# Kernel tuning notes

Measured on AMD Instinct MI355X. Metric: run time of the kernel, lower is better.

Reference implementation:

```python
import jax, jax.numpy as jnp
import numpy as np

N_NODES = 20000
IN_CH = 512
HEADS = 8
CH = 64  # hidden_layer per head
E = 320000
E_LABEL = 100000


def setup_inputs() -> dict:
    key = jax.random.key(0)
    ks = jax.random.split(key, 8)
    x = jax.random.normal(ks[0], (N_NODES, IN_CH), dtype=jnp.float32)
    edge_index = jax.random.randint(ks[1], (2, E), 0, N_NODES)
    edge_label_index = jax.random.randint(ks[2], (2, E_LABEL), 0, N_NODES)
    # GATv2Conv params (share_weights=False, bias=True)
    sc = 1.0 / np.sqrt(IN_CH)
    W_l = jax.random.normal(ks[3], (IN_CH, HEADS * CH), dtype=jnp.float32) * sc
    W_r = jax.random.normal(ks[4], (IN_CH, HEADS * CH), dtype=jnp.float32) * sc
    att = jax.random.normal(ks[5], (HEADS, CH), dtype=jnp.float32) * (1.0 / np.sqrt(CH))
    bias = jnp.zeros((HEADS * CH,), dtype=jnp.float32)
    gamma = jnp.ones((HEADS * CH,), dtype=jnp.float32)
    beta = jnp.zeros((HEADS * CH,), dtype=jnp.float32)
    return {"x": x, "edge_index": edge_index, "edge_label_index": edge_label_index,
            "W_l": W_l, "W_r": W_r, "att": att, "bias": bias,
            "gamma": gamma, "beta": beta}


def reference(x, edge_index, edge_label_index, W_l, W_r, att, bias, gamma, beta):
    N = x.shape[0]
    H, C = att.shape
    src, dst = edge_index[0], edge_index[1]
    # GATv2Conv: separate source/target linear maps
    xl = (x @ W_l).reshape(N, H, C)
    xr = (x @ W_r).reshape(N, H, C)
    # per-edge attention logits (GATv2: leaky_relu BEFORE attention vector)
    e = jax.nn.leaky_relu(xl[src] + xr[dst], negative_slope=0.2)  # [E,H,C]
    alpha = jnp.einsum('ehc,hc->eh', e, att)                      # [E,H]
    # softmax over incoming edges of each destination node
    amax = jax.ops.segment_max(alpha, dst, num_segments=N)        # [N,H]
    alpha = jnp.exp(alpha - amax[dst])
    denom = jax.ops.segment_sum(alpha, dst, num_segments=N)       # [N,H]
    alpha = alpha / (denom[dst] + 1e-16)
    # scatter-add aggregation of attended source messages
    out = jax.ops.segment_sum(alpha[:, :, None] * xl[src], dst, num_segments=N)  # [N,H,C]
    out = out.reshape(N, H * C) + bias
    # BatchNorm1d (training-mode batch stats, eps=1e-5)
    mu = out.mean(axis=0)
    var = out.var(axis=0)
    out = (out - mu) * jax.lax.rsqrt(var + 1e-5) * gamma + beta
    out = jax.nn.relu(out)  # dropout is identity in deterministic reference
    # gather + dot-product link scoring
    s = out[edge_label_index[0]]
    t = out[edge_label_index[1]]
    return jnp.sum(s * t, axis=1)  # [E_LABEL]
```

## Files before the change

kernel.cpp:

```cpp
#include <hip/hip_runtime.h>
#include <hip/hip_bf16.h>
#include <cstdint>

#define IN_CH 512
#define HC    512
#define HEADS 8
#define NPACK 1024

typedef __attribute__((ext_vector_type(8))) short bf16x8;
typedef __attribute__((ext_vector_type(8))) ushort u16x8;
typedef __attribute__((ext_vector_type(4))) float f32x4;
typedef __attribute__((ext_vector_type(2))) float f32x2;
typedef const __attribute__((address_space(1))) uint8_t* gaddr_t;
typedef __attribute__((address_space(3))) uint8_t* laddr_t;

__device__ inline ushort f2bf(float f) {
  uint32_t u = __float_as_uint(f);
  return (ushort)((u + 0x7fffu + ((u >> 16) & 1u)) >> 16);
}
__device__ inline float bf2f(ushort u) {
  return __uint_as_float(((uint32_t)u) << 16);
}

#if defined(__has_builtin)
#if __has_builtin(__builtin_amdgcn_cvt_pk_f32_fp8) && __has_builtin(__builtin_amdgcn_cvt_pk_fp8_f32)
#define HAVE_HW_FP8 1
#endif
#endif

__device__ __forceinline__ float fp8_decode_sw(uint32_t v) {
  const uint32_t t = v & 0x7fu;
  float m;
  if (t >= 8u) m = __uint_as_float((((t >> 3) + 120u) << 23) | ((t & 7u) << 20));
  else m = (float)t * 0.001953125f;
  return (v & 0x80u) ? -m : m;
}
__device__ __forceinline__ uint8_t fp8_encode_sw(float f) {
  const uint32_t b = __float_as_uint(f);
  const uint32_t s = (b >> 24) & 0x80u;
  uint32_t a = b & 0x7fffffffu;
  if (a >= 0x43e00000u) return (uint8_t)(s | 0x7eu);
  if (a < 0x3c800000u) {
    const int qi = (int)(__uint_as_float(a) * 512.0f + 0.5f);
    return (uint8_t)(s | (qi >= 8 ? 8u : (uint32_t)qi));
  }
  const uint32_t r = a + 0x7ffffu + ((a >> 20) & 1u);
  const uint32_t e = r >> 23;
  if (e > 135u) return (uint8_t)(s | 0x7eu);
  return (uint8_t)(s | ((e - 120u) << 3) | ((r >> 20) & 7u));
}

__device__ __forceinline__ void fp8x2_to_f32(uint32_t u, float& f0, float& f1, bool hi) {
#ifdef HAVE_HW_FP8
  const f32x2 p = hi ? __builtin_amdgcn_cvt_pk_f32_fp8(u, true)
                     : __builtin_amdgcn_cvt_pk_f32_fp8(u, false);
  f0 = p.x; f1 = p.y;
#else
  const uint32_t w = hi ? (u >> 16) : u;
  f0 = fp8_decode_sw(w & 0xffu);
  f1 = fp8_decode_sw((w >> 8) & 0xffu);
#endif
}
__device__ __forceinline__ uint8_t f32_to_fp8(float f) {
#ifdef HAVE_HW_FP8
  return (uint8_t)(__builtin_amdgcn_cvt_pk_fp8_f32(f, f, 0, false) & 0xff);
#else
  return fp8_encode_sw(f);
#endif
}

template<int CTRL>
__device__ __forceinline__ float dpp_add(float s) {
  const int t = __builtin_amdgcn_update_dpp(0, __float_as_int(s), CTRL, 0xf, 0xf, true);
  return s + __int_as_float(t);
}

__global__ void prep(const float* __restrict__ x, ushort* __restrict__ xb,
                     const float* __restrict__ Wl, const float* __restrict__ Wr,
                     ushort* __restrict__ bt,
                     const int* __restrict__ ei, int* __restrict__ counts,
                     const int* __restrict__ eli, int* __restrict__ counts2,
                     int n4, int E, int EL, int nbc, int nbp, int nbh) {
  const int b = blockIdx.x;
  if (b < nbc) {
    const int i = b * 256 + threadIdx.x;
    if (i < n4) {
      const float4 v = ((const float4*)x)[i];
      ushort4 o;
      o.x = f2bf(v.x); o.y = f2bf(v.y); o.z = f2bf(v.z); o.w = f2bf(v.w);
      ((ushort4*)xb)[i] = o;
    }
  } else if (b < nbc + nbp) {
    const int i = (b - nbc) * 256 + threadIdx.x;
    if (i < NPACK * IN_CH) {
      const int n = i >> 9, k = i & 511;
      const float v = (n < HC) ? Wl[(size_t)k * HC + n] : Wr[(size_t)k * HC + (n - HC)];
      bt[i] = f2bf(v);
    }
  } else if (b < nbc + nbp + nbh) {
    const int e = (b - nbc - nbp) * 256 + threadIdx.x;
    if (e < E) atomicAdd(&counts[ei[E + e]], 1);
  } else {
    const int e = (b - nbc - nbp - nbh) * 256 + threadIdx.x;
    if (e < EL) atomicAdd(&counts2[eli[e]], 1);
  }
}

__global__ __launch_bounds__(256) void gemm_mfma(
    const ushort* __restrict__ xb, const ushort* __restrict__ bt,
    uint8_t* __restrict__ xl8, ushort* __restrict__ xrb, int M) {
  __shared__ __align__(16) ushort As[128 * 32];
  __shared__ __align__(16) ushort Bs[128 * 32];
  const int wave = threadIdx.x >> 6, lane = threadIdx.x & 63;
  const int row0 = blockIdx.y * 128, col0 = blockIdx.x * 128;
  const int quad = lane >> 4, m16 = lane & 15;
  const int wrow = (wave >> 1) * 64, wcol = (wave & 1) * 64;
  const int srow = lane >> 2;
  const int scol = (lane & 3) * 8;
  const f32x4 zero = {0.f, 0.f, 0.f, 0.f};
  f32x4 acc[4][4];
  #pragma unroll
  for (int i = 0; i < 4; ++i)
    #pragma unroll
    for (int j = 0; j < 4; ++j) acc[i][j] = zero;

  for (int k0 = 0; k0 < IN_CH; k0 += 32) {
    #pragma unroll
    for (int c = 0; c < 2; ++c) {
      const int chunk = wave * 2 + c;
      const ushort* ga = xb + (size_t)(row0 + chunk * 16 + srow) * IN_CH + k0 + scol;
      __builtin_amdgcn_global_load_lds((gaddr_t)ga, (laddr_t)(As + chunk * 512), 16, 0, 0);
      const ushort* gb = bt + (size_t)(col0 + chunk * 16 + srow) * IN_CH + k0 + scol;
      __builtin_amdgcn_global_load_lds((gaddr_t)gb, (laddr_t)(Bs + chunk * 512), 16, 0, 0);
    }
    __syncthreads();
    bf16x8 af[4], bfr[4];
    #pragma unroll
    for (int i = 0; i < 4; ++i)
      af[i] = *(const bf16x8*)(As + (wrow + i * 16 + m16) * 32 + quad * 8);
    #pragma unroll
    for (int j = 0; j < 4; ++j)
      bfr[j] = *(const bf16x8*)(Bs + (wcol + j * 16 + m16) * 32 + quad * 8);
    #pragma unroll
    for (int i = 0; i < 4; ++i)
      #pragma unroll
      for (int j = 0; j < 4; ++j)
        acc[i][j] = __builtin_amdgcn_mfma_f32_16x16x32_bf16(af[i], bfr[j], acc[i][j], 0, 0, 0);
    __syncthreads();
  }
  const bool isL = (col0 < HC);
  if (isL) {
    #pragma unroll
    for (int i = 0; i < 4; ++i) {
      const int r = row0 + wrow + i * 16 + quad * 4;
      #pragma unroll
      for (int j = 0; j < 4; ++j) {
        const int cg = col0 + wcol + j * 16 + m16;
        #pragma unroll
        for (int t = 0; t < 4; ++t) {
          const int rr = r + t;
          if (rr < M) xl8[(size_t)rr * HC + cg] = f32_to_fp8(acc[i][j][t]);
        }
      }
    }
  } else {
    const int cbase = col0 - HC;
    #pragma unroll
    for (int i = 0; i < 4; ++i) {
      const int r = row0 + wrow + i * 16 + quad * 4;
      #pragma unroll
      for (int j = 0; j < 4; ++j) {
        const int cg = cbase + wcol + j * 16 + m16;
        #pragma unroll
        for (int t = 0; t < 4; ++t) {
          const int rr = r + t;
          if (rr < M) xrb[(size_t)rr * HC + cg] = f2bf(acc[i][j][t]);
        }
      }
    }
  }
}

__global__ __launch_bounds__(256) void scan_fused(
    const int* __restrict__ cA, int* __restrict__ oA, int* __restrict__ curA,
    int* __restrict__ fA,
    const int* __restrict__ cB, int* __restrict__ oB, int* __restrict__ curB,
    int* __restrict__ fB, int Nn, int nb) {
  const int half = (blockIdx.x >= nb) ? 1 : 0;
  const int blk  = blockIdx.x - half * nb;
  const int* counts = half ? cB : cA;
  int* offsets = half ? oB : oA;
  int* cursor  = half ? curB : curA;
  int* flags   = half ? fB : fA;
  __shared__ int tmp[256];
  __shared__ int sPref;
  const int t = threadIdx.x;
  const int i = blk * 256 + t;
  const int v = (i < Nn) ? counts[i] : 0;
  tmp[t] = v;
  __syncthreads();
  for (int d = 1; d < 256; d <<= 1) {
    int add = (t >= d) ? tmp[t - d] : 0;
    __syncthreads();
    tmp[t] += add;
    __syncthreads();
  }
  if (t == 0) atomicExch(&flags[blk], tmp[255] + 1);
  if (t < 64) {
    int s = 0;
    for (int b = t; b < blk; b += 64) {
      int f;
      do { f = atomicOr(&flags[b], 0); } while (f == 0);
      s += f - 1;
    }
    #pragma unroll
    for (int off = 32; off > 0; off >>= 1) s += __shfl_down(s, off, 64);
    if (t == 0) sPref = s;
  }
  __syncthreads();
  const int pref = sPref;
  if (i < Nn) {
    const int o = tmp[t] - v + pref;
    offsets[i] = o;
    cursor[i] = o;
  }
}

__global__ void csr_fill(const int* __restrict__ ei, int* __restrict__ cursor,
                         int* __restrict__ csr_src,
                         const int* __restrict__ eli, int* __restrict__ cursor2,
                         int* __restrict__ csr_t, int* __restrict__ csr_eid,
                         int E, int EL, int nbE) {
  const int b = blockIdx.x;
  if (b < nbE) {
    const int e = b * 256 + threadIdx.x;
    if (e < E) {
      const int pos = atomicAdd(&cursor[ei[E + e]], 1);
      csr_src[pos] = ei[e];
    }
  } else {
    const int e = (b - nbE) * 256 + threadIdx.x;
    if (e < EL) {
      const int pos = atomicAdd(&cursor2[eli[e]], 1);
      csr_t[pos] = eli[EL + e];
      csr_eid[pos] = e;
    }
  }
}

__global__ __launch_bounds__(256) void gatv2_agg(
    const uint8_t* __restrict__ xl8, const ushort* xrb, const float* __restrict__ att,
    const int* __restrict__ offsets, const int* __restrict__ counts,
    const int* __restrict__ csr_src, ushort* agg, int Nn) {
  const int node = blockIdx.x * 4 + (threadIdx.x >> 6);
  const int lane = threadIdx.x & 63;
  if (node >= Nn) return;
  const int start = offsets[node];
  const int deg   = counts[node];
  float rv[8], tv[8];
  {
    const u16x8 ur = *(const u16x8*)(xrb + (size_t)node * HC + lane * 8);
    #pragma unroll
    for (int c = 0; c < 8; ++c) rv[c] = bf2f((ushort)ur[c]);
    const float4* pa = (const float4*)(att + lane * 8);
    const float4 t0 = pa[0], t1 = pa[1];
    tv[0]=t0.x; tv[1]=t0.y; tv[2]=t0.z; tv[3]=t0.w;
    tv[4]=t1.x; tv[5]=t1.y; tv[6]=t1.z; tv[7]=t1.w;
  }
  float acc[8] = {};
  float densum = 0.f;
  const int* ps = csr_src + start;
  auto row = [&](int idx) {
    return *(const uint2*)(xl8 + (size_t)ps[idx] * HC + lane * 8);
  };
  auto body = [&](const uint2 cur) {
    float a[8];
    fp8x2_to_f32(cur.x, a[0], a[1], false);
    fp8x2_to_f32(cur.x, a[2], a[3], true);
    fp8x2_to_f32(cur.y, a[4], a[5], false);
    fp8x2_to_f32(cur.y, a[6], a[7], true);
    float s0 = 0.f, s1 = 0.f;
    #pragma unroll
    for (int c = 0; c < 4; ++c) {
      const float v = a[c] + rv[c];
      s0 += fmaxf(v, 0.2f * v) * tv[c];
    }
    #pragma unroll
    for (int c = 4; c < 8; ++c) {
      const float v = a[c] + rv[c];
      s1 += fmaxf(v, 0.2f * v) * tv[c];
    }
    float s = s0 + s1;
    s = dpp_add<0xB1>(s);
    s = dpp_add<0x4E>(s);
    s = dpp_add<0x141>(s);
    const float ea = __expf(s);
    densum += ea;
    #pragma unroll
    for (int c = 0; c < 8; ++c) acc[c] += ea * a[c];
  };

  uint2 b0 = {}, b1 = {};
  if (deg > 0) b0 = row(0);
  if (deg > 1) b1 = row(1);
  int i = 0;
  for (; i + 2 <= deg; i += 2) {
    const uint2 c0 = b0;
    if (i + 2 < deg) b0 = row(i + 2);
    const uint2 c1 = b1;
    if (i + 3 < deg) b1 = row(i + 3);
    body(c0);
    body(c1);
  }
  if (i < deg) body(b0);

  const float inv = 1.0f / (densum + 1e-16f);
  ushort* pd = agg + (size_t)node * HC + lane * 8;
  ushort4 o0, o1;
  o0.x = f2bf(acc[0] * inv); o0.y = f2bf(acc[1] * inv);
  o0.z = f2bf(acc[2] * inv); o0.w = f2bf(acc[3] * inv);
  o1.x = f2bf(acc[4] * inv); o1.y = f2bf(acc[5] * inv);
  o1.z = f2bf(acc[6] * inv); o1.w = f2bf(acc[7] * inv);
  *(ushort4*)(pd + 0) = o0;
  *(ushort4*)(pd + 4) = o1;
}

__global__ void bn_stats(const ushort* __restrict__ agg, float* __restrict__ gsum,
                         float* __restrict__ gsq, int* __restrict__ ctr,
                         const float* __restrict__ gamma, const float* __restrict__ beta,
                         float* __restrict__ aScale, float* __restrict__ bShift,
                         float invN, int Nn) {
  const int t = threadIdx.x;
  const int rows_per_block = (Nn + gridDim.x - 1) / gridDim.x;
  const int r0 = blockIdx.x * rows_per_block;
  const int r1 = min(Nn, r0 + rows_per_block);
  float s0 = 0.f, s1 = 0.f, q0 = 0.f, q1 = 0.f;
  for (int r = r0; r < r1; ++r) {
    const ushort2 u = ((const ushort2*)(agg + (size_t)r * HC))[t];
    const float v0 = bf2f(u.x), v1 = bf2f(u.y);
    s0 += v0; q0 += v0 * v0;
    s1 += v1; q1 += v1 * v1;
  }
  atomicAdd(&gsum[2 * t], s0);
  atomicAdd(&gsum[2 * t + 1], s1);
  atomicAdd(&gsq[2 * t], q0);
  atomicAdd(&gsq[2 * t + 1], q1);
  __shared__ int isLast;
  __syncthreads();
  if (t == 0) {
    __threadfence();
    isLast = (atomicAdd(ctr, 1) == (int)gridDim.x - 1) ? 1 : 0;
  }
  __syncthreads();
  if (isLast) {
    #pragma unroll
    for (int k = 0; k < 2; ++k) {
      const int c = t + k * 256;
      const float sum = atomicAdd(&gsum[c], 0.0f);
      const float sq  = atomicAdd(&gsq[c], 0.0f);
      const float m = sum * invN;
      const float var = sq * invN - m * m;
      const float rs = rsqrtf(var + 1e-5f);
      const float a = rs * gamma[c];
      aScale[c] = a;
      bShift[c] = beta[c] - m * a;
    }
  }
}

__global__ __launch_bounds__(256) void score_g(
    const ushort* __restrict__ agg, const float* __restrict__ aScale,
    const float* __restrict__ bShift, const int* __restrict__ off2,
    const int* __restrict__ cnt2, const int* __restrict__ csr_t,
    const int* __restrict__ csr_eid, float* __restrict__ out, int Nn) {
  const int node = blockIdx.x * 4 + (threadIdx.x >> 6);
  const int lane = threadIdx.x & 63;
  if (node >= Nn) return;
  const int start = off2[node];
  const int deg   = cnt2[node];
  if (deg == 0) return;
  float aS[8], bS[8], ys[8];
  {
    const float4* pa = (const float4*)(aScale + lane * 8);
    const float4 a0 = pa[0], a1 = pa[1];
    aS[0]=a0.x; aS[1]=a0.y; aS[2]=a0.z; aS[3]=a0.w;
    aS[4]=a1.x; aS[5]=a1.y; aS[6]=a1.z; aS[7]=a1.w;
    const float4* pb = (const float4*)(bShift + lane * 8);
    const float4 c0 = pb[0], c1 = pb[1];
    bS[0]=c0.x; bS[1]=c0.y; bS[2]=c0.z; bS[3]=c0.w;
    bS[4]=c1.x; bS[5]=c1.y; bS[6]=c1.z; bS[7]=c1.w;
    const u16x8 us = *(const u16x8*)(agg + (size_t)node * HC + lane * 8);
    #pragma unroll
    for (int c = 0; c < 8; ++c)
      ys[c] = fmaxf(0.f, bf2f((ushort)us[c]) * aS[c] + bS[c]);
  }
  const int* pt = csr_t + start;
  const int* pe = csr_eid + start;
  auto row = [&](int idx) {
    return *(const u16x8*)(agg + (size_t)pt[idx] * HC + lane * 8);
  };
  auto emit = [&](const u16x8 ut, int eid) {
    float s0 = 0.f, s1 = 0.f;
    #pragma unroll
    for (int c = 0; c < 4; ++c)
      s0 += ys[c] * fmaxf(0.f, bf2f((ushort)ut[c]) * aS[c] + bS[c]);
    #pragma unroll
    for (int c = 4; c < 8; ++c)
      s1 += ys[c] * fmaxf(0.f, bf2f((ushort)ut[c]) * aS[c] + bS[c]);
    float s = s0 + s1;
    s = dpp_add<0xB1>(s);
    s = dpp_add<0x4E>(s);
    s = dpp_add<0x141>(s);
    s = dpp_add<0x140>(s);
    s = dpp_add<0x142>(s);
    s = dpp_add<0x143>(s);
    if (lane == 63) out[eid] = s;
  };
  u16x8 b0 = {}, b1 = {};
  b0 = row(0);
  if (deg > 1) b1 = row(1);
  int j = 0;
  for (; j + 2 <= deg; j += 2) {
    const u16x8 c0 = b0;
    if (j + 2 < deg) b0 = row(j + 2);
    const u16x8 c1 = b1;
    if (j + 3 < deg) b1 = row(j + 3);
    emit(c0, pe[j]);
    emit(c1, pe[j + 1]);
  }
  if (j < deg) emit(b0, pe[j]);
}

extern "C" void kernel_launch(void* const* d_in, const int* in_sizes, int n_in,
                              void* d_out, int out_size, void* d_ws, size_t ws_size,
                              hipStream_t stream) {
  const float* x     = (const float*)d_in[0];
  const int*   ei    = (const int*)d_in[1];
  const int*   eli   = (const int*)d_in[2];
  const float* W_l   = (const float*)d_in[3];
  const float* W_r   = (const float*)d_in[4];
  const float* att   = (const float*)d_in[5];
  const float* gamma = (const float*)d_in[7];
  const float* beta  = (const float*)d_in[8];
  float* out = (float*)d_out;

  const int Nn = in_sizes[0] / IN_CH;
  const int E  = in_sizes[1] / 2;
  const int EL = in_sizes[2] / 2;

  uint8_t* xl8 = (uint8_t*)d_ws;
  ushort* xrb = (ushort*)d_ws + (size_t)Nn * HC;
  ushort* xbf = xrb + (size_t)Nn * HC;
  ushort* btb = xbf + (size_t)Nn * IN_CH;
  int* counts   = (int*)(btb + (size_t)NPACK * IN_CH);
  int* counts2  = counts + Nn;
  float* gsum   = (float*)(counts2 + Nn);
  float* gsq    = gsum + HC;
  int* flagsA   = (int*)(gsq + HC);
  int* flagsB   = flagsA + 128;
  int* bnctr    = flagsB + 128;
  int* offsets  = bnctr + 64;
  int* cursor   = offsets + Nn;
  int* offsets2 = cursor + Nn;
  int* cursor2  = offsets2 + Nn;
  int* csr_src  = cursor2 + Nn;
  int* csr_t    = csr_src + E;
  int* csr_eid  = csr_t + EL;
  float* aScale = (float*)(csr_eid + EL);
  float* bShift = aScale + HC;
  ushort* agg = xrb;

  const int nb  = (Nn + 255) / 256;
  const int nbc = (Nn * IN_CH / 4 + 255) / 256;
  const int nbp = (NPACK * IN_CH + 255) / 256;
  const int nbh = (E + 255) / 256;
  const int nbh2 = (EL + 255) / 256;

  (void)hipMemsetAsync(counts, 0, (2 * (size_t)Nn + 2 * HC + 320) * sizeof(int), stream);

  prep<<<nbc + nbp + nbh + nbh2, 256, 0, stream>>>(
      x, xbf, W_l, W_r, btb, ei, counts, eli, counts2,
      Nn * IN_CH / 4, E, EL, nbc, nbp, nbh);

  dim3 ggrid(NPACK / 128, (Nn + 127) / 128);
  gemm_mfma<<<ggrid, 256, 0, stream>>>(xbf, btb, xl8, xrb, Nn);

  scan_fused<<<2 * nb, 256, 0, stream>>>(counts, offsets, cursor, flagsA,
                                         counts2, offsets2, cursor2, flagsB, Nn, nb);
  csr_fill<<<nbh + nbh2, 256, 0, stream>>>(ei, cursor, csr_src,
                                           eli, cursor2, csr_t, csr_eid, E, EL, nbh);

  gatv2_agg<<<(Nn + 3) / 4, 256, 0, stream>>>(xl8, xrb, att, offsets, counts,
                                              csr_src, agg, Nn);

  bn_stats<<<200, 256, 0, stream>>>(agg, gsum, gsq, bnctr, gamma, beta,
                                    aScale, bShift, 1.0f / (float)Nn, Nn);

  score_g<<<(Nn + 3) / 4, 256, 0, stream>>>(agg, aScale, bShift, offsets2,
                                            counts2, csr_t, csr_eid, out, Nn);
}
```

Baseline: 292.8 us.

## Multi-buffer GEMM LDS tiles with 4-stage global_load_lds prefetch pipeline

Replaces the single-buffered K loop in the MFMA GEMM with a 4-slot LDS ring. Tiles are prefetched three steps ahead using direct global-to-LDS loads, and explicit vmcnt waits plus one barrier per step replace the two __syncthreads. The aim is to overlap global memory latency with MFMA work. It raises LDS use from 16KB to 64KB per block, which can lower occupancy, and its correctness depends on the hand-counted vmcnt values matching the four loads each stage issues.

```diff
diff --git a/kernel.cpp b/kernel.cpp
--- a/kernel.cpp
+++ b/kernel.cpp
@@ -109,8 +109,8 @@
 __global__ __launch_bounds__(256) void gemm_mfma(
     const ushort* __restrict__ xb, const ushort* __restrict__ bt,
     uint8_t* __restrict__ xl8, ushort* __restrict__ xrb, int M) {
-  __shared__ __align__(16) ushort As[128 * 32];
-  __shared__ __align__(16) ushort Bs[128 * 32];
+  __shared__ __align__(16) ushort As[4][128 * 32];
+  __shared__ __align__(16) ushort Bs[4][128 * 32];
   const int wave = threadIdx.x >> 6, lane = threadIdx.x & 63;
   const int row0 = blockIdx.y * 128, col0 = blockIdx.x * 128;
   const int quad = lane >> 4, m16 = lane & 15;
@@ -124,30 +124,49 @@
     #pragma unroll
     for (int j = 0; j < 4; ++j) acc[i][j] = zero;
 
-  for (int k0 = 0; k0 < IN_CH; k0 += 32) {
+  auto stage = [&](int buf, int kt) {
+    const int k0 = kt * 32;
     #pragma unroll
     for (int c = 0; c < 2; ++c) {
       const int chunk = wave * 2 + c;
       const ushort* ga = xb + (size_t)(row0 + chunk * 16 + srow) * IN_CH + k0 + scol;
-      __builtin_amdgcn_global_load_lds((gaddr_t)ga, (laddr_t)(As + chunk * 512), 16, 0, 0);
+      __builtin_amdgcn_global_load_lds((gaddr_t)ga, (laddr_t)(&As[buf][chunk * 512]), 16, 0, 0);
       const ushort* gb = bt + (size_t)(col0 + chunk * 16 + srow) * IN_CH + k0 + scol;
-      __builtin_amdgcn_global_load_lds((gaddr_t)gb, (laddr_t)(Bs + chunk * 512), 16, 0, 0);
-    }
-    __syncthreads();
+      __builtin_amdgcn_global_load_lds((gaddr_t)gb, (laddr_t)(&Bs[buf][chunk * 512]), 16, 0, 0);
+    }
+  };
+  auto compute = [&](int buf) {
     bf16x8 af[4], bfr[4];
     #pragma unroll
     for (int i = 0; i < 4; ++i)
-      af[i] = *(const bf16x8*)(As + (wrow + i * 16 + m16) * 32 + quad * 8);
+      af[i] = *(const bf16x8*)(&As[buf][(wrow + i * 16 + m16) * 32 + quad * 8]);
     #pragma unroll
     for (int j = 0; j < 4; ++j)
-      bfr[j] = *(const bf16x8*)(Bs + (wcol + j * 16 + m16) * 32 + quad * 8);
+      bfr[j] = *(const bf16x8*)(&Bs[buf][(wcol + j * 16 + m16) * 32 + quad * 8]);
     #pragma unroll
     for (int i = 0; i < 4; ++i)
       #pragma unroll
       for (int j = 0; j < 4; ++j)
         acc[i][j] = __builtin_amdgcn_mfma_f32_16x16x32_bf16(af[i], bfr[j], acc[i][j], 0, 0, 0);
-    __syncthreads();
-  }
+  };
+
+  stage(0, 0); stage(1, 1); stage(2, 2);
+  for (int kt = 0; kt <= 12; ++kt) {
+    asm volatile("s_waitcnt vmcnt(8)" ::: "memory");
+    __builtin_amdgcn_s_barrier();
+    stage((kt + 3) & 3, kt + 3);
+    compute(kt & 3);
+  }
+  asm volatile("s_waitcnt vmcnt(8)" ::: "memory");
+  __builtin_amdgcn_s_barrier();
+  compute(13 & 3);
+  asm volatile("s_waitcnt vmcnt(4)" ::: "memory");
+  __builtin_amdgcn_s_barrier();
+  compute(14 & 3);
+  asm volatile("s_waitcnt vmcnt(0)" ::: "memory");
+  __builtin_amdgcn_s_barrier();
+  compute(15 & 3);
+
   const bool isL = (col0 < HC);
   if (isL) {
     #pragma unroll
```

After: 291.6 us. Within noise of the previous version (-0.4%).
